# Kernel optimization log

Hardware: AMD Instinct MI355X
Metric: run time of the kernel (lower is better)

Reference implementation:

```python
import jax, jax.numpy as jnp
import numpy as np

N1, N2, D, F = 8192, 8192, 1024, 800


def setup_inputs() -> dict:
    key = jax.random.key(0)
    ks = jax.random.split(key, 10)
    s = 1.0 / np.sqrt(D)
    return {
        "m1": jax.random.normal(ks[0], (N1, D), jnp.float32),
        "m2": jax.random.normal(ks[1], (N2, D), jnp.float32),
        "Wf1": jax.random.normal(ks[2], (F, D), jnp.float32) * s,
        "bf1": jax.random.normal(ks[3], (F,), jnp.float32) * 0.01,
        "Wf2": jax.random.normal(ks[4], (F, D), jnp.float32) * s,
        "bf2": jax.random.normal(ks[5], (F,), jnp.float32) * 0.01,
        "W1": jax.random.normal(ks[6], (F, D), jnp.float32) * s,
        "b1": jax.random.normal(ks[7], (F,), jnp.float32) * 0.01,
        "W2": jax.random.normal(ks[8], (F, D), jnp.float32) * s,
        "b2": jax.random.normal(ks[9], (F,), jnp.float32) * 0.01,
    }


def reference(m1, m2, Wf1, bf1, Wf2, bf2, W1, b1, W2, b2):
    # raw_prod: [N1, N2]
    raw = jnp.einsum('id,jd->ij', m1, m2)
    alpha2 = jax.nn.softmax(raw, axis=-1)        # rows over m2: [N1, N2]
    alpha1 = jax.nn.softmax(raw.T, axis=-1)      # rows over m1: [N2, N1]
    attended_m1 = alpha1 @ m1                    # [N2, D]
    attended_m2 = alpha2 @ m2                    # [N1, D]
    # eval mode: dropout is identity
    filter1 = jax.nn.sigmoid((attended_m2 @ Wf1.T + bf1).mean(0))  # [F]
    filter2 = jax.nn.sigmoid((attended_m1 @ Wf2.T + bf2).mean(0))  # [F]
    transformed_m1 = jnp.tanh(attended_m1 @ W1.T + b1).mean(0)     # [F]
    transformed_m2 = jnp.tanh(attended_m2 @ W2.T + b2).mean(0)     # [F]
    return (transformed_m1 * filter1, transformed_m2 * filter2)
```

## Files before the change

kernel.cpp:

```cpp
#include <hip/hip_runtime.h>

typedef __attribute__((ext_vector_type(8))) short s8v;
typedef __attribute__((ext_vector_type(4))) float f4v;
typedef __attribute__((ext_vector_type(4))) unsigned short us4v;
typedef __attribute__((ext_vector_type(8))) unsigned short us8v;
typedef _Float16 h8v __attribute__((ext_vector_type(8)));

#define MFMA(a, b, c) __builtin_amdgcn_mfma_f32_16x16x32_bf16(a, b, c, 0, 0, 0)
#define GLOAD16(g, l)                                                          \
  __builtin_amdgcn_global_load_lds((const __attribute__((address_space(1))) void*)(g), \
                                   (__attribute__((address_space(3))) void*)(l), 16, 0, 0)

#define L2E 1.44269504088896f

__device__ __forceinline__ unsigned short f2bf(float x) {
  unsigned int u = __float_as_uint(x);
  u += 0x7fffu + ((u >> 16) & 1u);
  return (unsigned short)(u >> 16);
}
__device__ __forceinline__ float bf2f(unsigned short h) {
  return __uint_as_float(((unsigned int)h) << 16);
}
__device__ __forceinline__ float f16bits2f(unsigned short u) {
  union { unsigned short us; _Float16 f; } cv; cv.us = u; return (float)cv.f;
}

__global__ void k_zero(float* p, int n) {
  int i = blockIdx.x * 256 + threadIdx.x;
  if (i < n) p[i] = 0.f;
}

__global__ __launch_bounds__(256) void k_wbf(const float* __restrict__ W,
                                             unsigned short* __restrict__ wb) {
  int idx = blockIdx.x * 256 + threadIdx.x;
  int f = idx >> 10;
  wb[idx] = f2bf((f < 800) ? W[idx] : 0.f);
}

__global__ __launch_bounds__(256) void k_prep(const float* __restrict__ in,
                                              unsigned short* __restrict__ outb,
                                              unsigned short* __restrict__ outT) {
  __shared__ float lf[64 * 68];
  int bx = blockIdx.x;
  int rb = bx >> 4, cb = bx & 15;
  long r0 = (long)rb * 64, c0 = (long)cb * 64;
  int tid = threadIdx.x;
#pragma unroll
  for (int q = 0; q < 4; ++q) {
    int fid = tid + 256 * q;
    int r = fid >> 4, c4 = fid & 15;
    f4v v = *(const f4v*)&in[(r0 + r) * 1024 + c0 + 4 * c4];
    *(f4v*)&lf[r * 68 + 4 * c4] = v;
    us4v h;
#pragma unroll
    for (int e = 0; e < 4; ++e) h[e] = f2bf(v[e]);
    *(us4v*)&outb[(r0 + r) * 1024 + c0 + 4 * c4] = h;
  }
  __syncthreads();
#pragma unroll
  for (int q = 0; q < 4; ++q) {
    int fid = tid + 256 * q;
    int oc = fid >> 4, or4 = fid & 15;
    us4v h;
#pragma unroll
    for (int e = 0; e < 4; ++e) h[e] = f2bf(lf[(4 * or4 + e) * 68 + oc]);
    *(us4v*)&outT[(c0 + oc) * 8192 + r0 + 4 * or4] = h;
  }
}

__global__ __launch_bounds__(512, 2) void k_gemm_raw8(const unsigned short* __restrict__ m1b,
                                                      const unsigned short* __restrict__ m2b,
                                                      _Float16* __restrict__ rawh) {
  __shared__ unsigned short LDS[65536];
  const int tid = threadIdx.x, lane = tid & 63, wid = tid >> 6;
  const int wr = wid >> 2, wc = wid & 3;
  const int x = lane >> 4;

  int swz = ((int)blockIdx.x & 7) * 128 + ((int)blockIdx.x >> 3);
  const long i0 = (long)(swz >> 5) * 256;
  const long j0 = (long)(swz & 31) * 256;

  const unsigned short* gA[4];
  const unsigned short* gB[4];
  int ldst[4];
#pragma unroll
  for (int s = 0; s < 4; ++s) {
    int c = s * 512 + tid;
    int r = c >> 3, qp = c & 7;
    int ql = qp ^ (r & 7);
    gA[s] = m1b + (i0 + r) * 1024 + ql * 8;
    gB[s] = m2b + (j0 + r) * 1024 + ql * 8;
    ldst[s] = c * 8;
  }
  int offA[2][8], offB[2][4];
#pragma unroll
  for (int kk = 0; kk < 2; ++kk) {
#pragma unroll
    for (int m = 0; m < 8; ++m) {
      int rr = wr * 128 + m * 16 + (lane & 15);
      offA[kk][m] = (rr * 8 + ((kk * 4 + x) ^ (rr & 7))) * 8;
    }
#pragma unroll
    for (int n = 0; n < 4; ++n) {
      int cc = wc * 64 + n * 16 + (lane & 15);
      offB[kk][n] = (cc * 8 + ((kk * 4 + x) ^ (cc & 7))) * 8;
    }
  }

  f4v acc[8][4];
#pragma unroll
  for (int m = 0; m < 8; ++m)
#pragma unroll
    for (int n = 0; n < 4; ++n) acc[m][n] = (f4v)0.f;

#define STAGE8(b, kt)                                                         \
  do {                                                                        \
    _Pragma("unroll") for (int s = 0; s < 4; ++s)                             \
        GLOAD16(gA[s] + (kt) * 64, &LDS[(b) * 32768 + ldst[s]]);              \
    _Pragma("unroll") for (int s = 0; s < 4; ++s)                             \
        GLOAD16(gB[s] + (kt) * 64, &LDS[(b) * 32768 + 16384 + ldst[s]]);      \
  } while (0)

  STAGE8(0, 0);
  STAGE8(1, 1);

  for (int kt = 0; kt < 16; ++kt) {
    const int b = kt & 1;
    if (kt < 15) asm volatile("s_waitcnt vmcnt(8)" ::: "memory");
    else         asm volatile("s_waitcnt vmcnt(0)" ::: "memory");
    asm volatile("s_barrier" ::: "memory");
    __builtin_amdgcn_sched_barrier(0);
    const int Ab = b * 32768, Bb = b * 32768 + 16384;
#pragma unroll
    for (int kk = 0; kk < 2; ++kk) {
      s8v af[8], bf[4];
#pragma unroll
      for (int m = 0; m < 8; ++m) af[m] = *(const s8v*)&LDS[Ab + offA[kk][m]];
#pragma unroll
      for (int n = 0; n < 4; ++n) bf[n] = *(const s8v*)&LDS[Bb + offB[kk][n]];
      __builtin_amdgcn_s_setprio(1);
#pragma unroll
      for (int m = 0; m < 8; ++m)
#pragma unroll
        for (int n = 0; n < 4; ++n)
          acc[m][n] = MFMA(af[m], bf[n], acc[m][n]);
      __builtin_amdgcn_s_setprio(0);
    }
    asm volatile("s_barrier" ::: "memory");
    __builtin_amdgcn_sched_barrier(0);
    if (kt < 14) STAGE8(b, kt + 2);
  }
#undef STAGE8

#pragma unroll
  for (int m = 0; m < 8; ++m) {
    long rbase = i0 + wr * 128 + m * 16 + x * 4;
#pragma unroll
    for (int n = 0; n < 4; ++n) {
      long col = j0 + wc * 64 + n * 16 + (lane & 15);
#pragma unroll
      for (int r = 0; r < 4; ++r) rawh[(rbase + r) * 8192 + col] = (_Float16)acc[m][n][r];
    }
  }
}

__global__ __launch_bounds__(512, 2) void k_gemm_att8(const unsigned short* __restrict__ P,
                                                      const unsigned short* __restrict__ BT,
                                                      unsigned short* __restrict__ attb,
                                                      float* __restrict__ meanv) {
  __shared__ unsigned short LDS[49152];
  const int tid = threadIdx.x, lane = tid & 63, wid = tid >> 6;
  const int wr = wid >> 1, wc = wid & 1;
  const int x = lane >> 4;

  int swz = ((int)blockIdx.x & 7) * 32 + ((int)blockIdx.x >> 3);
  const long i0 = (long)(swz >> 3) * 256;
  const long d0 = (long)(swz & 7) * 128;

  const unsigned short* gA[4];
  const unsigned short* gB[2];
  int ldstA[4], ldstB[2];
#pragma unroll
  for (int s = 0; s < 4; ++s) {
    int c = s * 512 + tid;
    int r = c >> 3, qp = c & 7;
    int ql = qp ^ (r & 7);
    gA[s] = P + (i0 + r) * 8192 + ql * 8;
    ldstA[s] = c * 8;
  }
#pragma unroll
  for (int s = 0; s < 2; ++s) {
    int c = s * 512 + tid;
    int r = c >> 3, qp = c & 7;
    int ql = qp ^ (r & 7);
    gB[s] = BT + (d0 + r) * 8192 + ql * 8;
    ldstB[s] = c * 8;
  }
  int offA[2][4], offB[2][4];
#pragma unroll
  for (int kk = 0; kk < 2; ++kk) {
#pragma unroll
    for (int m = 0; m < 4; ++m) {
      int rr = wr * 64 + m * 16 + (lane & 15);
      offA[kk][m] = (rr * 8 + ((kk * 4 + x) ^ (rr & 7))) * 8;
    }
#pragma unroll
    for (int n = 0; n < 4; ++n) {
      int cc = wc * 64 + n * 16 + (lane & 15);
      offB[kk][n] = (cc * 8 + ((kk * 4 + x) ^ (cc & 7))) * 8;
    }
  }

  f4v acc[4][4];
#pragma unroll
  for (int m = 0; m < 4; ++m)
#pragma unroll
    for (int n = 0; n < 4; ++n) acc[m][n] = (f4v)0.f;

#define STAGEA(b, kt)                                                         \
  do {                                                                        \
    _Pragma("unroll") for (int s = 0; s < 4; ++s)                             \
        GLOAD16(gA[s] + (kt) * 64, &LDS[(b) * 24576 + ldstA[s]]);             \
    _Pragma("unroll") for (int s = 0; s < 2; ++s)                             \
        GLOAD16(gB[s] + (kt) * 64, &LDS[(b) * 24576 + 16384 + ldstB[s]]);     \
  } while (0)

  STAGEA(0, 0);
  STAGEA(1, 1);

  for (int kt = 0; kt < 128; ++kt) {
    const int b = kt & 1;
    if (kt < 127) asm volatile("s_waitcnt vmcnt(6)" ::: "memory");
    else          asm volatile("s_waitcnt vmcnt(0)" ::: "memory");
    asm volatile("s_barrier" ::: "memory");
    __builtin_amdgcn_sched_barrier(0);
    const int Ab = b * 24576, Bb = b * 24576 + 16384;
#pragma unroll
    for (int kk = 0; kk < 2; ++kk) {
      s8v af[4], bf[4];
#pragma unroll
      for (int m = 0; m < 4; ++m) af[m] = *(const s8v*)&LDS[Ab + offA[kk][m]];
#pragma unroll
      for (int n = 0; n < 4; ++n) bf[n] = *(const s8v*)&LDS[Bb + offB[kk][n]];
      __builtin_amdgcn_s_setprio(1);
#pragma unroll
      for (int m = 0; m < 4; ++m)
#pragma unroll
        for (int n = 0; n < 4; ++n)
          acc[m][n] = MFMA(af[m], bf[n], acc[m][n]);
      __builtin_amdgcn_s_setprio(0);
    }
    asm volatile("s_barrier" ::: "memory");
    __builtin_amdgcn_sched_barrier(0);
    if (kt < 126) STAGEA(b, kt + 2);
  }
#undef STAGEA

#pragma unroll
  for (int n = 0; n < 4; ++n) {
    long colg = d0 + wc * 64 + n * 16 + (lane & 15);
    float s = 0.f;
#pragma unroll
    for (int m = 0; m < 4; ++m) {
      long rowg = i0 + wr * 64 + m * 16 + x * 4;
      f4v a = acc[m][n];
#pragma unroll
      for (int r = 0; r < 4; ++r) {
        attb[(rowg + r) * 1024 + colg] = f2bf(a[r]);
        s += a[r];
      }
    }
    s += __shfl_xor(s, 16);
    s += __shfl_xor(s, 32);
    if (lane < 16) atomicAdd(&meanv[d0 + wc * 64 + n * 16 + lane], s);
  }
}

__global__ __launch_bounds__(256) void k_rowstats(const _Float16* __restrict__ rawh,
                                                  float* __restrict__ rm2) {
  const long i = blockIdx.x;
  const int tid = threadIdx.x, lane = tid & 63, wv = tid >> 6;
  const h8v* r8 = (const h8v*)(rawh + i * 8192);
  h8v v[4];
  float m = -3.4e38f;
#pragma unroll
  for (int q = 0; q < 4; ++q) {
    v[q] = r8[tid + 256 * q];
#pragma unroll
    for (int e = 0; e < 8; ++e) m = fmaxf(m, (float)v[q][e]);
  }
#pragma unroll
  for (int off = 32; off >= 1; off >>= 1) m = fmaxf(m, __shfl_xor(m, off));
  __shared__ float sm[4], ss[4];
  if (lane == 0) sm[wv] = m;
  __syncthreads();
  m = fmaxf(fmaxf(sm[0], sm[1]), fmaxf(sm[2], sm[3]));
  float s = 0.f;
#pragma unroll
  for (int q = 0; q < 4; ++q)
#pragma unroll
    for (int e = 0; e < 8; ++e) s += __expf((float)v[q][e] - m);
#pragma unroll
  for (int off = 32; off >= 1; off >>= 1) s += __shfl_xor(s, off);
  if (lane == 0) ss[wv] = s;
  __syncthreads();
  if (tid == 0) rm2[i] = fmaf(m, L2E, log2f(ss[0] + ss[1] + ss[2] + ss[3]));
}

__global__ __launch_bounds__(256) void k_colpart(const _Float16* __restrict__ rawh,
                                                 float* __restrict__ cpm,
                                                 float* __restrict__ cps) {
  int bx = blockIdx.x;
  int cb = bx & 31, ib = bx >> 5;
  long j = (long)cb * 256 + threadIdx.x;
  float m = -3.4e38f, s = 0.f;
  for (int r = 0; r < 256; ++r) {
    float v = (float)rawh[(long)(ib * 256 + r) * 8192 + j];
    float nm = fmaxf(m, v);
    s = s * __expf(m - nm) + __expf(v - nm);
    m = nm;
  }
  cpm[(long)ib * 8192 + j] = m;
  cps[(long)ib * 8192 + j] = s;
}

__global__ __launch_bounds__(256) void k_colcomb(const float* __restrict__ cpm,
                                                 const float* __restrict__ cps,
                                                 float* __restrict__ hh) {
  long j = (long)blockIdx.x * 256 + threadIdx.x;
  float m = -3.4e38f, s = 0.f;
  for (int c = 0; c < 32; ++c) {
    float pm = cpm[(long)c * 8192 + j];
    float ps = cps[(long)c * 8192 + j];
    float nm = fmaxf(m, pm);
    s = s * __expf(m - nm) + ps * __expf(pm - nm);
    m = nm;
  }
  hh[j] = fmaf(m, L2E, log2f(s));
}

__global__ __launch_bounds__(256) void k_texp_ip(unsigned short* buf,
                                                 const float* __restrict__ hh) {
  __shared__ unsigned short lt[2][64 * 80];
  int a = blockIdx.x >> 7, b = blockIdx.x & 127;
  if (a > b) return;
  const int tid = threadIdx.x;
  const int r = tid & 63;
  const int cw = tid >> 6;
  const int ntile = (a == b) ? 1 : 2;

  for (int t = 0; t < ntile; ++t) {
    long ro = (long)(t == 0 ? a : b) * 64;
    long co = (long)(t == 0 ? b : a) * 64;
#pragma unroll
    for (int q = 0; q < 2; ++q) {
      int c8 = cw + 4 * q;
      us8v u = *(const us8v*)&buf[(ro + r) * 8192 + co + c8 * 8];
      f4v hA = *(const f4v*)&hh[co + c8 * 8];
      f4v hB = *(const f4v*)&hh[co + c8 * 8 + 4];
#pragma unroll
      for (int e = 0; e < 8; ++e) {
        float hv = (e < 4) ? hA[e] : hB[e - 4];
        lt[t][(c8 * 8 + e) * 80 + r] = f2bf(exp2f(fmaf(f16bits2f(u[e]), L2E, -hv)));
      }
    }
  }
  __syncthreads();
  for (int t = 0; t < ntile; ++t) {
    long dr = (long)(t == 0 ? b : a) * 64;
    long dc = (long)(t == 0 ? a : b) * 64;
#pragma unroll
    for (int q = 0; q < 2; ++q) {
      int fid = tid + 256 * q;
      int jr = fid >> 3, c8 = fid & 7;
      us8v o = *(const us8v*)&lt[t][jr * 80 + c8 * 8];
      *(us8v*)&buf[(dr + jr) * 8192 + dc + c8 * 8] = o;
    }
  }
}

__global__ __launch_bounds__(256) void k_prow_ip(unsigned short* buf,
                                                 const float* __restrict__ hh,
                                                 const float* __restrict__ rm2) {
  __shared__ unsigned short lt[2][64 * 80];
  int a = blockIdx.x >> 7, b = blockIdx.x & 127;
  if (a > b) return;
  const int tid = threadIdx.x;
  const int r = tid & 63;
  const int cw = tid >> 6;
  const int ntile = (a == b) ? 1 : 2;

  for (int t = 0; t < ntile; ++t) {
    long ro = (long)(t == 0 ? a : b) * 64;
    long co = (long)(t == 0 ? b : a) * 64;
    float hj;
#pragma unroll
    for (int q = 0; q < 2; ++q) {
      int c8 = cw + 4 * q;
      us8v u = *(const us8v*)&buf[(ro + r) * 8192 + co + c8 * 8];
      if (q == 0) hj = hh[ro + r];
      f4v rA = *(const f4v*)&rm2[co + c8 * 8];
      f4v rB = *(const f4v*)&rm2[co + c8 * 8 + 4];
#pragma unroll
      for (int e = 0; e < 8; ++e) {
        float rv = (e < 4) ? rA[e] : rB[e - 4];
        float sc = exp2f(fminf(hj - rv, 120.f));
        lt[t][(c8 * 8 + e) * 80 + r] = f2bf(bf2f(u[e]) * sc);
      }
    }
  }
  __syncthreads();
  for (int t = 0; t < ntile; ++t) {
    long dr = (long)(t == 0 ? b : a) * 64;
    long dc = (long)(t == 0 ? a : b) * 64;
#pragma unroll
    for (int q = 0; q < 2; ++q) {
      int fid = tid + 256 * q;
      int ir = fid >> 3, c8 = fid & 7;
      us8v o = *(const us8v*)&lt[t][ir * 80 + c8 * 8];
      *(us8v*)&buf[(dr + ir) * 8192 + dc + c8 * 8] = o;
    }
  }
}

__global__ __launch_bounds__(256) void k_gemm_tanh(const unsigned short* __restrict__ attb,
                                                   const unsigned short* __restrict__ Wb,
                                                   const float* __restrict__ bias,
                                                   float* __restrict__ acct) {
  __shared__ unsigned short As[128 * 32], Bs[128 * 32];
  const int tid = threadIdx.x, lane = tid & 63, wv = tid >> 6;
  const int wrow = wv >> 1, wcol = wv & 1;
  int sw = ((int)blockIdx.x & 7) * 56 + ((int)blockIdx.x >> 3);
  const long i0 = (long)(sw / 7) * 128;
  const long f0 = (long)(sw % 7) * 128;

  const int r16 = lane >> 2;
  const int sslot = (lane & 3) ^ ((r16 >> 1) & 3);
  const unsigned short* gA0 = &attb[(i0 + 32 * wv + r16) * 1024 + sslot * 8];
  const unsigned short* gA1 = gA0 + 16 * 1024;
  const unsigned short* gB0 = &Wb[(f0 + 32 * wv + r16) * 1024 + sslot * 8];
  const unsigned short* gB1 = gB0 + 16 * 1024;
  unsigned short* lA0 = &As[(32 * wv) * 32];
  unsigned short* lA1 = &As[(32 * wv + 16) * 32];
  unsigned short* lB0 = &Bs[(32 * wv) * 32];
  unsigned short* lB1 = &Bs[(32 * wv + 16) * 32];

  f4v acc[4][4];
#pragma unroll
  for (int a = 0; a < 4; ++a)
#pragma unroll
    for (int b = 0; b < 4; ++b) acc[a][b] = (f4v)0.f;

  for (int kt = 0; kt < 32; ++kt) {
    GLOAD16(gA0 + kt * 32, lA0);
    GLOAD16(gA1 + kt * 32, lA1);
    GLOAD16(gB0 + kt * 32, lB0);
    GLOAD16(gB1 + kt * 32, lB1);
    __syncthreads();
    const int kkx = lane >> 4;
    s8v af[4], bf[4];
#pragma unroll
    for (int mf = 0; mf < 4; ++mf) {
      int rr = wrow * 64 + mf * 16 + (lane & 15);
      af[mf] = *(const s8v*)&As[rr * 32 + (kkx ^ ((rr >> 1) & 3)) * 8];
      int cc = wcol * 64 + mf * 16 + (lane & 15);
      bf[mf] = *(const s8v*)&Bs[cc * 32 + (kkx ^ ((cc >> 1) & 3)) * 8];
    }
#pragma unroll
    for (int mf = 0; mf < 4; ++mf)
#pragma unroll
      for (int nf = 0; nf < 4; ++nf)
        acc[mf][nf] = MFMA(af[mf], bf[nf], acc[mf][nf]);
    __syncthreads();
  }
#pragma unroll
  for (int nf = 0; nf < 4; ++nf) {
    long colg = f0 + wcol * 64 + nf * 16 + (lane & 15);
    float bv = (colg < 800) ? bias[colg] : 0.f;
    float s = 0.f;
#pragma unroll
    for (int mf = 0; mf < 4; ++mf) {
      f4v a = acc[mf][nf];
#pragma unroll
      for (int r = 0; r < 4; ++r) s += tanhf(a[r] + bv);
    }
    s += __shfl_xor(s, 16);
    s += __shfl_xor(s, 32);
    if (lane < 16) atomicAdd(&acct[f0 + wcol * 64 + nf * 16 + lane], s);
  }
}

__global__ __launch_bounds__(256) void k_filt(const float* __restrict__ Wf1,
                                              const float* __restrict__ bf1,
                                              const float* __restrict__ Wf2,
                                              const float* __restrict__ bf2,
                                              const float* __restrict__ mean2,
                                              const float* __restrict__ mean1,
                                              float* __restrict__ filt1,
                                              float* __restrict__ filt2) {
  int wv = threadIdx.x >> 6, lane = threadIdx.x & 63;
  int gid = blockIdx.x * 4 + wv;
  const float* Wr;
  const float* mv;
  float b;
  float* outp;
  if (gid < 800) {
    Wr = Wf1 + (long)gid * 1024; mv = mean2; b = bf1[gid]; outp = filt1 + gid;
  } else {
    int f = gid - 800;
    Wr = Wf2 + (long)f * 1024; mv = mean1; b = bf2[f]; outp = filt2 + f;
  }
  float s = 0.f;
#pragma unroll
  for (int q = 0; q < 16; ++q) s += mv[lane + 64 * q] * Wr[lane + 64 * q];
#pragma unroll
  for (int off = 32; off >= 1; off >>= 1) s += __shfl_xor(s, off);
  if (lane == 0) *outp = 1.f / (1.f + __expf(-(s * (1.f / 8192.f) + b)));
}

__global__ void k_final(const float* __restrict__ acct1, const float* __restrict__ acct2,
                        const float* __restrict__ filt1, const float* __restrict__ filt2,
                        float* __restrict__ out) {
  int i = blockIdx.x * 256 + threadIdx.x;
  if (i < 800) {
    out[i] = acct1[i] * (1.f / 8192.f) * filt1[i];
    out[800 + i] = acct2[i] * (1.f / 8192.f) * filt2[i];
  }
}

extern "C" void kernel_launch(void* const* d_in, const int* in_sizes, int n_in,
                              void* d_out, int out_size, void* d_ws, size_t ws_size,
                              hipStream_t stream) {
  (void)in_sizes; (void)n_in; (void)out_size;
  const float* m1  = (const float*)d_in[0];
  const float* m2  = (const float*)d_in[1];
  const float* Wf1 = (const float*)d_in[2];
  const float* bf1 = (const float*)d_in[3];
  const float* Wf2 = (const float*)d_in[4];
  const float* bf2 = (const float*)d_in[5];
  const float* W1  = (const float*)d_in[6];
  const float* b1  = (const float*)d_in[7];
  const float* W2  = (const float*)d_in[8];
  const float* b2  = (const float*)d_in[9];
  float* out = (float*)d_out;
  char* ws = (char*)d_ws;

  _Float16* rawh       = (_Float16*)(ws);
  unsigned short* rawu = (unsigned short*)(ws);
  unsigned short* m1T  = (unsigned short*)(ws + 134217728UL);
  unsigned short* m2T  = (unsigned short*)(ws + 150994944UL);
  unsigned short* m1b  = (unsigned short*)(ws + 167772160UL);
  unsigned short* m2b  = (unsigned short*)(ws + 184549376UL);
  unsigned short* att1 = (unsigned short*)(ws + 167772160UL);
  unsigned short* att2 = (unsigned short*)(ws + 184549376UL);
  unsigned short* W1b  = (unsigned short*)(ws + 201326592UL);
  unsigned short* W2b  = (unsigned short*)(ws + 203161600UL);
  float* rm2   = (float*)(ws + 204996608UL);
  float* hh    = (float*)(ws + 205062144UL);
  float* cpm   = (float*)(ws + 205127680UL);
  float* cps   = (float*)(ws + 206176256UL);
  float* mean1 = (float*)(ws + 207224832UL);
  float* mean2 = (float*)(ws + 207228928UL);
  float* acct1 = (float*)(ws + 207233024UL);
  float* acct2 = (float*)(ws + 207236608UL);
  float* filt1 = (float*)(ws + 207240192UL);
  float* filt2 = (float*)(ws + 207243392UL);

  if (ws_size < 207246592UL) return;

  k_zero<<<15, 256, 0, stream>>>(mean1, 3840);
  k_wbf<<<3584, 256, 0, stream>>>(W1, W1b);
  k_wbf<<<3584, 256, 0, stream>>>(W2, W2b);
  k_prep<<<2048, 256, 0, stream>>>(m1, m1b, m1T);
  k_prep<<<2048, 256, 0, stream>>>(m2, m2b, m2T);
  k_gemm_raw8<<<1024, 512, 0, stream>>>(m1b, m2b, rawh);
  k_rowstats<<<8192, 256, 0, stream>>>(rawh, rm2);
  k_colpart<<<1024, 256, 0, stream>>>(rawh, cpm, cps);
  k_colcomb<<<32, 256, 0, stream>>>(cpm, cps, hh);
  k_texp_ip<<<16384, 256, 0, stream>>>(rawu, hh);
  k_gemm_att8<<<256, 512, 0, stream>>>(rawu, m1T, att1, mean1);
  k_prow_ip<<<16384, 256, 0, stream>>>(rawu, hh, rm2);
  k_gemm_att8<<<256, 512, 0, stream>>>(rawu, m2T, att2, mean2);
  k_gemm_tanh<<<448, 256, 0, stream>>>(att1, W1b, b1, acct1);
  k_gemm_tanh<<<448, 256, 0, stream>>>(att2, W2b, b2, acct2);
  k_filt<<<400, 256, 0, stream>>>(Wf1, bf1, Wf2, bf2, mean2, mean1, filt1, filt2);
  k_final<<<4, 256, 0, stream>>>(acct1, acct2, filt1, filt2, out);
}
```

Before: 662.9 us.

## Use four-stage BK=32 LDS ring with one barrier per k-step in both GEMMs

Both bf16 MFMA GEMM kernels move from a double-buffered K=64 tile with two barriers per iteration to a four-slot ring of K=32 tiles, with three tiles in flight. Fragments are read from LDS first, then the next global-to-LDS load is issued into the free slot, so the second barrier can be dropped. The XOR swizzle is changed to match the 4-chunk rows. The aim is deeper prefetch and less barrier stall. In exchange there are twice as many iterations and barriers per unit of K, and fewer MFMAs per barrier.

```diff
diff --git a/kernel.cpp b/kernel.cpp
--- a/kernel.cpp
+++ b/kernel.cpp
@@ -80,31 +80,28 @@
   const long i0 = (long)(swz >> 5) * 256;
   const long j0 = (long)(swz & 31) * 256;
 
-  const unsigned short* gA[4];
-  const unsigned short* gB[4];
-  int ldst[4];
-#pragma unroll
-  for (int s = 0; s < 4; ++s) {
+  const unsigned short* gA[2];
+  const unsigned short* gB[2];
+  int ldst[2];
+#pragma unroll
+  for (int s = 0; s < 2; ++s) {
     int c = s * 512 + tid;
-    int r = c >> 3, qp = c & 7;
-    int ql = qp ^ (r & 7);
+    int r = c >> 2, qp = c & 3;
+    int ql = qp ^ ((r >> 1) & 3);
     gA[s] = m1b + (i0 + r) * 1024 + ql * 8;
     gB[s] = m2b + (j0 + r) * 1024 + ql * 8;
     ldst[s] = c * 8;
   }
-  int offA[2][8], offB[2][4];
-#pragma unroll
-  for (int kk = 0; kk < 2; ++kk) {
-#pragma unroll
-    for (int m = 0; m < 8; ++m) {
-      int rr = wr * 128 + m * 16 + (lane & 15);
-      offA[kk][m] = (rr * 8 + ((kk * 4 + x) ^ (rr & 7))) * 8;
-    }
-#pragma unroll
-    for (int n = 0; n < 4; ++n) {
-      int cc = wc * 64 + n * 16 + (lane & 15);
-      offB[kk][n] = (cc * 8 + ((kk * 4 + x) ^ (cc & 7))) * 8;
-    }
+  int offA[8], offB[4];
+#pragma unroll
+  for (int m = 0; m < 8; ++m) {
+    int rr = wr * 128 + m * 16 + (lane & 15);
+    offA[m] = (rr * 4 + (x ^ ((rr >> 1) & 3))) * 8;
+  }
+#pragma unroll
+  for (int n = 0; n < 4; ++n) {
+    int cc = wc * 64 + n * 16 + (lane & 15);
+    offB[n] = (cc * 4 + (x ^ ((cc >> 1) & 3))) * 8;
   }
 
   f4v acc[8][4];
@@ -113,44 +110,41 @@
 #pragma unroll
     for (int n = 0; n < 4; ++n) acc[m][n] = (f4v)0.f;
 
-#define STAGE8(b, kt)                                                         \
+#define STG(u, kt)                                                            \
   do {                                                                        \
-    _Pragma("unroll") for (int s = 0; s < 4; ++s)                             \
-        GLOAD16(gA[s] + (kt) * 64, &LDS[(b) * 32768 + ldst[s]]);              \
-    _Pragma("unroll") for (int s = 0; s < 4; ++s)                             \
-        GLOAD16(gB[s] + (kt) * 64, &LDS[(b) * 32768 + 16384 + ldst[s]]);      \
+    _Pragma("unroll") for (int s = 0; s < 2; ++s)                             \
+        GLOAD16(gA[s] + (kt) * 32, &LDS[(u) * 16384 + ldst[s]]);              \
+    _Pragma("unroll") for (int s = 0; s < 2; ++s)                             \
+        GLOAD16(gB[s] + (kt) * 32, &LDS[(u) * 16384 + 8192 + ldst[s]]);       \
   } while (0)
 
-  STAGE8(0, 0);
-  STAGE8(1, 1);
-
-  for (int kt = 0; kt < 16; ++kt) {
-    const int b = kt & 1;
-    if (kt < 15) asm volatile("s_waitcnt vmcnt(8)" ::: "memory");
-    else         asm volatile("s_waitcnt vmcnt(0)" ::: "memory");
+  STG(0, 0); STG(1, 1); STG(2, 2);
+
+  for (int kt = 0; kt < 32; ++kt) {
+    const int u = kt & 3;
+    if (kt < 30)      asm volatile("s_waitcnt vmcnt(8)" ::: "memory");
+    else if (kt == 30) asm volatile("s_waitcnt vmcnt(4)" ::: "memory");
+    else               asm volatile("s_waitcnt vmcnt(0)" ::: "memory");
     asm volatile("s_barrier" ::: "memory");
     __builtin_amdgcn_sched_barrier(0);
-    const int Ab = b * 32768, Bb = b * 32768 + 16384;
-#pragma unroll
-    for (int kk = 0; kk < 2; ++kk) {
-      s8v af[8], bf[4];
-#pragma unroll
-      for (int m = 0; m < 8; ++m) af[m] = *(const s8v*)&LDS[Ab + offA[kk][m]];
-#pragma unroll
-      for (int n = 0; n < 4; ++n) bf[n] = *(const s8v*)&LDS[Bb + offB[kk][n]];
-      __builtin_amdgcn_s_setprio(1);
-#pragma unroll
-      for (int m = 0; m < 8; ++m)
-#pragma unroll
-        for (int n = 0; n < 4; ++n)
-          acc[m][n] = MFMA(af[m], bf[n], acc[m][n]);
-      __builtin_amdgcn_s_setprio(0);
-    }
-    asm volatile("s_barrier" ::: "memory");
+    const int Ab = u * 16384, Bb = u * 16384 + 8192;
+    s8v af[8], bf[4];
+#pragma unroll
+    for (int m = 0; m < 8; ++m) af[m] = *(const s8v*)&LDS[Ab + offA[m]];
+#pragma unroll
+    for (int n = 0; n < 4; ++n) bf[n] = *(const s8v*)&LDS[Bb + offB[n]];
+    if (kt < 29) STG((kt + 3) & 3, kt + 3);
+    asm volatile("s_waitcnt lgkmcnt(0)" ::: "memory");
     __builtin_amdgcn_sched_barrier(0);
-    if (kt < 14) STAGE8(b, kt + 2);
-  }
-#undef STAGE8
+    __builtin_amdgcn_s_setprio(1);
+#pragma unroll
+    for (int m = 0; m < 8; ++m)
+#pragma unroll
+      for (int n = 0; n < 4; ++n)
+        acc[m][n] = MFMA(af[m], bf[n], acc[m][n]);
+    __builtin_amdgcn_s_setprio(0);
+  }
+#undef STG
 
 #pragma unroll
   for (int m = 0; m < 8; ++m) {
@@ -177,38 +171,34 @@
   const long i0 = (long)(swz >> 3) * 256;
   const long d0 = (long)(swz & 7) * 128;
 
-  const unsigned short* gA[4];
-  const unsigned short* gB[2];
-  int ldstA[4], ldstB[2];
-#pragma unroll
-  for (int s = 0; s < 4; ++s) {
+  const unsigned short* gA[2];
+  const unsigned short* gB0;
+  int ldstA[2], ldstB0;
+#pragma unroll
+  for (int s = 0; s < 2; ++s) {
     int c = s * 512 + tid;
-    int r = c >> 3, qp = c & 7;
-    int ql = qp ^ (r & 7);
+    int r = c >> 2, qp = c & 3;
+    int ql = qp ^ ((r >> 1) & 3);
     gA[s] = P + (i0 + r) * 8192 + ql * 8;
     ldstA[s] = c * 8;
   }
-#pragma unroll
-  for (int s = 0; s < 2; ++s) {
-    int c = s * 512 + tid;
-    int r = c >> 3, qp = c & 7;
-    int ql = qp ^ (r & 7);
-    gB[s] = BT + (d0 + r) * 8192 + ql * 8;
-    ldstB[s] = c * 8;
-  }
-  int offA[2][4], offB[2][4];
-#pragma unroll
-  for (int kk = 0; kk < 2; ++kk) {
-#pragma unroll
-    for (int m = 0; m < 4; ++m) {
-      int rr = wr * 64 + m * 16 + (lane & 15);
-      offA[kk][m] = (rr * 8 + ((kk * 4 + x) ^ (rr & 7))) * 8;
-    }
-#pragma unroll
-    for (int n = 0; n < 4; ++n) {
-      int cc = wc * 64 + n * 16 + (lane & 15);
-      offB[kk][n] = (cc * 8 + ((kk * 4 + x) ^ (cc & 7))) * 8;
-    }
+  {
+    int c = tid;
+    int r = c >> 2, qp = c & 3;
+    int ql = qp ^ ((r >> 1) & 3);
+    gB0 = BT + (d0 + r) * 8192 + ql * 8;
+    ldstB0 = c * 8;
+  }
+  int offA[4], offB[4];
+#pragma unroll
+  for (int m = 0; m < 4; ++m) {
+    int rr = wr * 64 + m * 16 + (lane & 15);
+    offA[m] = (rr * 4 + (x ^ ((rr >> 1) & 3))) * 8;
+  }
+#pragma unroll
+  for (int n = 0; n < 4; ++n) {
+    int cc = wc * 64 + n * 16 + (lane & 15);
+    offB[n] = (cc * 4 + (x ^ ((cc >> 1) & 3))) * 8;
   }
 
   f4v acc[4][4];
@@ -217,44 +207,40 @@
 #pragma unroll
     for (int n = 0; n < 4; ++n) acc[m][n] = (f4v)0.f;
 
-#define STAGEA(b, kt)                                                         \
+#define STGA(u, kt)                                                           \
   do {                                                                        \
-    _Pragma("unroll") for (int s = 0; s < 4; ++s)                             \
-        GLOAD16(gA[s] + (kt) * 64, &LDS[(b) * 24576 + ldstA[s]]);             \
     _Pragma("unroll") for (int s = 0; s < 2; ++s)                             \
-        GLOAD16(gB[s] + (kt) * 64, &LDS[(b) * 24576 + 16384 + ldstB[s]]);     \
+        GLOAD16(gA[s] + (kt) * 32, &LDS[(u) * 12288 + ldstA[s]]);             \
+    GLOAD16(gB0 + (kt) * 32, &LDS[(u) * 12288 + 8192 + ldstB0]);              \
   } while (0)
 
-  STAGEA(0, 0);
-  STAGEA(1, 1);
-
-  for (int kt = 0; kt < 128; ++kt) {
-    const int b = kt & 1;
-    if (kt < 127) asm volatile("s_waitcnt vmcnt(6)" ::: "memory");
-    else          asm volatile("s_waitcnt vmcnt(0)" ::: "memory");
+  STGA(0, 0); STGA(1, 1); STGA(2, 2);
+
+  for (int kt = 0; kt < 256; ++kt) {
+    const int u = kt & 3;
+    if (kt < 254)       asm volatile("s_waitcnt vmcnt(6)" ::: "memory");
+    else if (kt == 254) asm volatile("s_waitcnt vmcnt(3)" ::: "memory");
+    else                asm volatile("s_waitcnt vmcnt(0)" ::: "memory");
     asm volatile("s_barrier" ::: "memory");
     __builtin_amdgcn_sched_barrier(0);
-    const int Ab = b * 24576, Bb = b * 24576 + 16384;
-#pragma unroll
-    for (int kk = 0; kk < 2; ++kk) {
-      s8v af[4], bf[4];
-#pragma unroll
-      for (int m = 0; m < 4; ++m) af[m] = *(const s8v*)&LDS[Ab + offA[kk][m]];
-#pragma unroll
-      for (int n = 0; n < 4; ++n) bf[n] = *(const s8v*)&LDS[Bb + offB[kk][n]];
-      __builtin_amdgcn_s_setprio(1);
-#pragma unroll
-      for (int m = 0; m < 4; ++m)
-#pragma unroll
-        for (int n = 0; n < 4; ++n)
-          acc[m][n] = MFMA(af[m], bf[n], acc[m][n]);
-      __builtin_amdgcn_s_setprio(0);
-    }
-    asm volatile("s_barrier" ::: "memory");
+    const int Ab = u * 12288, Bb = u * 12288 + 8192;
+    s8v af[4], bf[4];
+#pragma unroll
+    for (int m = 0; m < 4; ++m) af[m] = *(const s8v*)&LDS[Ab + offA[m]];
+#pragma unroll
+    for (int n = 0; n < 4; ++n) bf[n] = *(const s8v*)&LDS[Bb + offB[n]];
+    if (kt < 253) STGA((kt + 3) & 3, kt + 3);
+    asm volatile("s_waitcnt lgkmcnt(0)" ::: "memory");
     __builtin_amdgcn_sched_barrier(0);
-    if (kt < 126) STAGEA(b, kt + 2);
-  }
-#undef STAGEA
+    __builtin_amdgcn_s_setprio(1);
+#pragma unroll
+    for (int m = 0; m < 4; ++m)
+#pragma unroll
+      for (int n = 0; n < 4; ++n)
+        acc[m][n] = MFMA(af[m], bf[n], acc[m][n]);
+    __builtin_amdgcn_s_setprio(0);
+  }
+#undef STGA
 
 #pragma unroll
   for (int n = 0; n < 4; ++n) {
```

After: 642.1 us. 3.1% less time.
